# Kernel optimization log

Hardware: AMD Instinct MI355X
Metric: run time of the kernel (lower is better)

## Reference

```python
import jax, jax.numpy as jnp
import numpy as np

N_HEAD = 10

def setup_inputs() -> dict:
    key = jax.random.key(0)
    k1, k2, k3 = jax.random.split(key, 3)
    n_embd = 640
    x = jax.random.normal(k1, (4, 2048, n_embd), dtype=jnp.float32)
    w_qkv = jax.random.normal(k2, (3 * n_embd, n_embd), dtype=jnp.float32) * (1.0 / np.sqrt(n_embd))
    w_proj = jax.random.normal(k3, (n_embd, n_embd), dtype=jnp.float32) * (1.0 / np.sqrt(n_embd))
    return {"x": x, "w_qkv": w_qkv, "w_proj": w_proj}

def reference(x, w_qkv, w_proj):
    bsz, seqlen, n_embd = x.shape
    head_dim = n_embd // N_HEAD
    qkv = jnp.einsum('bsd,ed->bse', x, w_qkv)  # [B,S,3E]
    q, k, v = jnp.split(qkv, 3, axis=2)
    # [B,H,S,Dh]
    q = q.reshape(bsz, seqlen, N_HEAD, head_dim).transpose(0, 2, 1, 3)
    k = k.reshape(bsz, seqlen, N_HEAD, head_dim).transpose(0, 2, 1, 3)
    v = v.reshape(bsz, seqlen, N_HEAD, head_dim).transpose(0, 2, 1, 3)
    scale = 1.0 / np.sqrt(head_dim).astype(np.float32)
    scores = jnp.einsum('bhqd,bhkd->bhqk', q, k) * scale
    causal = jnp.tril(jnp.ones((seqlen, seqlen), dtype=bool))
    scores = jnp.where(causal, scores, jnp.finfo(scores.dtype).min)
    attn = jax.nn.softmax(scores, axis=-1)
    y = jnp.einsum('bhqk,bhkd->bhqd', attn, v)
    y = y.transpose(0, 2, 1, 3).reshape(bsz, seqlen, n_embd)
    return jnp.einsum('bsd,ed->bse', y, w_proj)
```

## Files before the change

kernel.cpp:

```cpp
#include <hip/hip_runtime.h>

#define BB 4
#define SS 2048
#define EE 640
#define NHH 10
#define DHH 64
#define MTOK 8192
#define E33 1920

#define LDST 72

#if __has_builtin(__builtin_amdgcn_exp2f)
#define EXP2(x) __builtin_amdgcn_exp2f(x)
#else
#define EXP2(x) exp2f(x)
#endif

#define QSCALE 0.18033688011112042f

typedef float f32x4 __attribute__((ext_vector_type(4)));
typedef __bf16 bf16x8 __attribute__((ext_vector_type(8)));
typedef __bf16 bf16x4 __attribute__((ext_vector_type(4)));
typedef unsigned short u16;
typedef u16 u16x4 __attribute__((ext_vector_type(4)));

__device__ inline u16 f2bf(float f) {
  unsigned u = __builtin_bit_cast(unsigned, f);
  u += 0x7fffu + ((u >> 16) & 1u);
  return (u16)(u >> 16);
}

#define XN4   1310720
#define WQN4   307200
#define WPN4   102400
__global__ void convert_all(const float* __restrict__ x, const float* __restrict__ wqkv,
                            const float* __restrict__ wproj,
                            u16* __restrict__ xb, u16* __restrict__ wqkvb,
                            u16* __restrict__ wprojb) {
  int i = blockIdx.x * blockDim.x + threadIdx.x;
  const float* src; u16* dst; int off;
  if (i < XN4)              { src = x;     dst = xb;     off = i; }
  else if (i < XN4 + WQN4)  { src = wqkv;  dst = wqkvb;  off = i - XN4; }
  else if (i < XN4 + WQN4 + WPN4) { src = wproj; dst = wprojb; off = i - XN4 - WQN4; }
  else return;
  float4 v = ((const float4*)src)[off];
  u16x4 o = { f2bf(v.x), f2bf(v.y), f2bf(v.z), f2bf(v.w) };
  ((u16x4*)dst)[off] = o;
}

__global__ __launch_bounds__(256) void gemm_qkv(
    const u16* __restrict__ A, const u16* __restrict__ Bt,
    u16* __restrict__ qb, u16* __restrict__ kb, u16* __restrict__ vt) {
  __shared__ __align__(16) u16 As[128 * LDST];
  __shared__ __align__(16) u16 Bs[128 * LDST];
  const int t = threadIdx.x;
  const int m0 = blockIdx.y * 128;
  const int n0 = blockIdx.x * 128;
  const int w = t >> 6, lane = t & 63, n16 = lane & 15, quad = lane >> 4;
  const int wm = w >> 1, wn = w & 1;

  f32x4 acc[4][4];
  for (int i = 0; i < 4; i++)
    for (int j = 0; j < 4; j++) acc[i][j] = f32x4{0.f, 0.f, 0.f, 0.f};

  bf16x8 pa[4], pb[4];
#pragma unroll
  for (int i = 0; i < 4; ++i) {
    int c = i * 256 + t, row = c >> 3, col0 = (c & 7) * 8;
    pa[i] = *(const bf16x8*)&A[(m0 + row) * 640 + col0];
    pb[i] = *(const bf16x8*)&Bt[(n0 + row) * 640 + col0];
  }

  for (int kt = 0; kt < 10; ++kt) {
    __syncthreads();
#pragma unroll
    for (int i = 0; i < 4; ++i) {
      int c = i * 256 + t, row = c >> 3, col0 = (c & 7) * 8;
      *(bf16x8*)&As[row * LDST + col0] = pa[i];
      *(bf16x8*)&Bs[row * LDST + col0] = pb[i];
    }
    __syncthreads();
    if (kt < 9) {
#pragma unroll
      for (int i = 0; i < 4; ++i) {
        int c = i * 256 + t, row = c >> 3, col0 = (c & 7) * 8;
        pa[i] = *(const bf16x8*)&A[(m0 + row) * 640 + (kt + 1) * 64 + col0];
        pb[i] = *(const bf16x8*)&Bt[(n0 + row) * 640 + (kt + 1) * 64 + col0];
      }
    }
#pragma unroll
    for (int ks = 0; ks < 2; ++ks) {
      bf16x8 a[4], b[4];
      for (int mi = 0; mi < 4; mi++)
        a[mi] = *(const bf16x8*)&As[(wm * 64 + mi * 16 + n16) * LDST + ks * 32 + quad * 8];
      for (int ni = 0; ni < 4; ni++)
        b[ni] = *(const bf16x8*)&Bs[(wn * 64 + ni * 16 + n16) * LDST + ks * 32 + quad * 8];
      for (int mi = 0; mi < 4; mi++)
        for (int ni = 0; ni < 4; ni++)
          acc[mi][ni] = __builtin_amdgcn_mfma_f32_16x16x32_bf16(a[mi], b[ni], acc[mi][ni], 0, 0, 0);
    }
  }

  const int which = n0 / 640;
  for (int ni = 0; ni < 4; ni++) {
    int col = n0 + wn * 64 + ni * 16 + n16;
    int eh = col - which * 640;
    int h = eh >> 6, d = eh & 63;
    for (int mi = 0; mi < 4; mi++) {
      int tb = m0 + wm * 64 + mi * 16 + quad * 4;
      f32x4 c = acc[mi][ni];
      if (which == 0) {
        c[0] *= QSCALE; c[1] *= QSCALE; c[2] *= QSCALE; c[3] *= QSCALE;
      }
      if (which == 2) {
        int b_ = tb >> 11, s_ = tb & 2047;
        u16x4 pk = { f2bf(c[0]), f2bf(c[1]), f2bf(c[2]), f2bf(c[3]) };
        *(u16x4*)&vt[((b_ * NHH + h) * DHH + d) * SS + s_] = pk;
      } else {
        u16* dst = (which == 0) ? qb : kb;
        for (int r = 0; r < 4; r++) {
          int tok = tb + r;
          int b_ = tok >> 11, s_ = tok & 2047;
          dst[((b_ * NHH + h) * SS + s_) * DHH + d] = f2bf(c[r]);
        }
      }
    }
  }
}

__global__ __launch_bounds__(256) void attn_kernel(
    const u16* __restrict__ qb, const u16* __restrict__ kb, const u16* __restrict__ vt,
    u16* __restrict__ y) {
  __shared__ __align__(16) u16 Ks[2][64 * LDST];
  __shared__ __align__(16) u16 Vs[2][64 * LDST];
  const int t = threadIdx.x;
  const int w = t >> 6, lane = t & 63, n16 = lane & 15, quad = lane >> 4;
  const int bh = blockIdx.x;
  const int qt = 31 - blockIdx.y;
  const int qb0 = qt * 64;
  const int b_ = bh / NHH, h = bh % NHH;

  bf16x8 aq[2];
  {
    const u16* qp = &qb[(bh * SS + qb0 + w * 16 + n16) * DHH];
    aq[0] = *(const bf16x8*)&qp[quad * 8];
    aq[1] = *(const bf16x8*)&qp[32 + quad * 8];
  }
  const int q_rel = w * 16 + n16;

  const int c1 = 256 + t;
  const int row0 = t >> 3,  col0 = (t & 7) * 8;
  const int row1 = c1 >> 3, col1 = (c1 & 7) * 8;
  auto perm = [](int k) {
    int p = k >> 5, rem = k & 31, qd = rem >> 3, tt = rem & 7;
    return ((p << 1) | (tt >> 2)) * 16 + qd * 4 + (tt & 3);
  };
  const int prow0 = perm(row0), prow1 = perm(row1);

  float4 fk0, fk1, fv0, fv1;
  fk0 = *(const float4*)&kb[(bh * SS + row0) * DHH + col0];
  fk1 = *(const float4*)&kb[(bh * SS + row1) * DHH + col1];
  fv0 = *(const float4*)&vt[(bh * DHH + row0) * SS + col0];
  fv1 = *(const float4*)&vt[(bh * DHH + row1) * SS + col1];
  *(float4*)&Ks[0][prow0 * LDST + col0] = fk0;
  *(float4*)&Ks[0][prow1 * LDST + col1] = fk1;
  *(float4*)&Vs[0][row0 * LDST + col0] = fv0;
  *(float4*)&Vs[0][row1 * LDST + col1] = fv1;

  float m_i = -1e30f, l_i = 0.f;
  f32x4 o[4];
  for (int db = 0; db < 4; db++) o[db] = f32x4{0.f, 0.f, 0.f, 0.f};

  for (int kt = 0; kt <= qt; ++kt) {
    __syncthreads();
    const int cur = kt & 1, nxt = cur ^ 1;
    if (kt < qt) {
      int kk = (kt + 1) * 64;
      fk0 = *(const float4*)&kb[(bh * SS + kk + row0) * DHH + col0];
      fk1 = *(const float4*)&kb[(bh * SS + kk + row1) * DHH + col1];
      fv0 = *(const float4*)&vt[(bh * DHH + row0) * SS + kk + col0];
      fv1 = *(const float4*)&vt[(bh * DHH + row1) * SS + kk + col1];
    }

    f32x4 sc[4];
#pragma unroll
    for (int nb = 0; nb < 4; nb++) {
      f32x4 c = f32x4{0.f, 0.f, 0.f, 0.f};
      bf16x8 ak0 = *(const bf16x8*)&Ks[cur][(nb * 16 + n16) * LDST + quad * 8];
      c = __builtin_amdgcn_mfma_f32_16x16x32_bf16(ak0, aq[0], c, 0, 0, 0);
      bf16x8 ak1 = *(const bf16x8*)&Ks[cur][(nb * 16 + n16) * LDST + 32 + quad * 8];
      c = __builtin_amdgcn_mfma_f32_16x16x32_bf16(ak1, aq[1], c, 0, 0, 0);
      sc[nb] = c;
    }

    if (kt == qt) {
#pragma unroll
      for (int nb = 0; nb < 4; nb++)
#pragma unroll
        for (int r = 0; r < 4; r++) {
          int key = ((nb >> 1) << 5) + quad * 8 + ((nb & 1) << 2) + r;
          if (key > q_rel) sc[nb][r] = -1e30f;
        }
    }

    f32x4 mx;
#pragma unroll
    for (int r = 0; r < 4; r++)
      mx[r] = fmaxf(fmaxf(sc[0][r], sc[1][r]), fmaxf(sc[2][r], sc[3][r]));
    float rm = fmaxf(fmaxf(mx[0], mx[1]), fmaxf(mx[2], mx[3]));
    rm = fmaxf(rm, __shfl_xor(rm, 16));
    rm = fmaxf(rm, __shfl_xor(rm, 32));

    if (!__all(rm - m_i <= 8.0f)) {
      float mnew = fmaxf(m_i, rm);
      float alpha = EXP2(m_i - mnew);
      l_i *= alpha;
#pragma unroll
      for (int db = 0; db < 4; db++)
#pragma unroll
        for (int r = 0; r < 4; r++) o[db][r] *= alpha;
      m_i = mnew;
    }

    f32x4 ps[4];
#pragma unroll
    for (int nb = 0; nb < 4; nb++)
#pragma unroll
      for (int r = 0; r < 4; r++) ps[nb][r] = EXP2(sc[nb][r] - m_i);
    f32x4 sv;
#pragma unroll
    for (int r = 0; r < 4; r++)
      sv[r] = (ps[0][r] + ps[1][r]) + (ps[2][r] + ps[3][r]);
    float rs = (sv[0] + sv[1]) + (sv[2] + sv[3]);
    rs += __shfl_xor(rs, 16);
    rs += __shfl_xor(rs, 32);
    l_i += rs;

#pragma unroll
    for (int p2 = 0; p2 < 2; p2++) {
      bf16x8 bp;
#pragma unroll
      for (int j = 0; j < 4; j++) {
        bp[j]     = (__bf16)ps[2 * p2][j];
        bp[4 + j] = (__bf16)ps[2 * p2 + 1][j];
      }
#pragma unroll
      for (int db = 0; db < 4; db++) {
        bf16x8 av = *(const bf16x8*)&Vs[cur][(db * 16 + n16) * LDST + p2 * 32 + quad * 8];
        o[db] = __builtin_amdgcn_mfma_f32_16x16x32_bf16(av, bp, o[db], 0, 0, 0);
      }
    }

    if (kt < qt) {
      *(float4*)&Ks[nxt][prow0 * LDST + col0] = fk0;
      *(float4*)&Ks[nxt][prow1 * LDST + col1] = fk1;
      *(float4*)&Vs[nxt][row0 * LDST + col0] = fv0;
      *(float4*)&Vs[nxt][row1 * LDST + col1] = fv1;
    }
  }

  const float inv = 1.0f / l_i;
  const int tok = b_ * SS + qb0 + w * 16 + n16;
#pragma unroll
  for (int db = 0; db < 4; db++) {
    bf16x4 pk = { (__bf16)(o[db][0] * inv), (__bf16)(o[db][1] * inv),
                  (__bf16)(o[db][2] * inv), (__bf16)(o[db][3] * inv) };
    *(bf16x4*)&y[tok * EE + h * DHH + db * 16 + quad * 4] = pk;
  }
}

__global__ __launch_bounds__(256) void gemm_proj(
    const u16* __restrict__ A, const u16* __restrict__ Bt, float* __restrict__ out) {
  __shared__ __align__(16) u16 As[128 * LDST];
  __shared__ __align__(16) u16 Bs[128 * LDST];
  const int t = threadIdx.x;
  const int m0 = blockIdx.y * 128;
  const int n0 = blockIdx.x * 128;
  const int w = t >> 6, lane = t & 63, n16 = lane & 15, quad = lane >> 4;
  const int wm = w >> 1, wn = w & 1;

  f32x4 acc[4][4];
  for (int i = 0; i < 4; i++)
    for (int j = 0; j < 4; j++) acc[i][j] = f32x4{0.f, 0.f, 0.f, 0.f};

  bf16x8 pa[4], pb[4];
#pragma unroll
  for (int i = 0; i < 4; ++i) {
    int c = i * 256 + t, row = c >> 3, col0 = (c & 7) * 8;
    pa[i] = *(const bf16x8*)&A[(m0 + row) * 640 + col0];
    pb[i] = *(const bf16x8*)&Bt[(n0 + row) * 640 + col0];
  }

  for (int kt = 0; kt < 10; ++kt) {
    __syncthreads();
#pragma unroll
    for (int i = 0; i < 4; ++i) {
      int c = i * 256 + t, row = c >> 3, col0 = (c & 7) * 8;
      *(bf16x8*)&As[row * LDST + col0] = pa[i];
      *(bf16x8*)&Bs[row * LDST + col0] = pb[i];
    }
    __syncthreads();
    if (kt < 9) {
#pragma unroll
      for (int i = 0; i < 4; ++i) {
        int c = i * 256 + t, row = c >> 3, col0 = (c & 7) * 8;
        pa[i] = *(const bf16x8*)&A[(m0 + row) * 640 + (kt + 1) * 64 + col0];
        pb[i] = *(const bf16x8*)&Bt[(n0 + row) * 640 + (kt + 1) * 64 + col0];
      }
    }
#pragma unroll
    for (int ks = 0; ks < 2; ++ks) {
      bf16x8 a[4], b[4];
      for (int mi = 0; mi < 4; mi++)
        a[mi] = *(const bf16x8*)&As[(wm * 64 + mi * 16 + n16) * LDST + ks * 32 + quad * 8];
      for (int ni = 0; ni < 4; ni++)
        b[ni] = *(const bf16x8*)&Bs[(wn * 64 + ni * 16 + n16) * LDST + ks * 32 + quad * 8];
      for (int mi = 0; mi < 4; mi++)
        for (int ni = 0; ni < 4; ni++)
          acc[mi][ni] = __builtin_amdgcn_mfma_f32_16x16x32_bf16(a[mi], b[ni], acc[mi][ni], 0, 0, 0);
    }
  }

  for (int ni = 0; ni < 4; ni++) {
    int col = n0 + wn * 64 + ni * 16 + n16;
    for (int mi = 0; mi < 4; mi++) {
      int rowb = m0 + wm * 64 + mi * 16 + quad * 4;
      f32x4 c = acc[mi][ni];
      for (int r = 0; r < 4; r++) out[(rowb + r) * 640 + col] = c[r];
    }
  }
}

extern "C" void kernel_launch(void* const* d_in, const int* in_sizes, int n_in,
                              void* d_out, int out_size, void* d_ws, size_t ws_size,
                              hipStream_t stream) {
  const float* x     = (const float*)d_in[0];
  const float* wqkv  = (const float*)d_in[1];
  const float* wproj = (const float*)d_in[2];
  float* out = (float*)d_out;

  char* ws = (char*)d_ws;
  u16* xb     = (u16*)(ws + 0);
  u16* wqkvb  = (u16*)(ws + 10485760);
  u16* wprojb = (u16*)(ws + 12943360);
  u16* qbuf   = (u16*)(ws + 13762560);
  u16* kbuf   = (u16*)(ws + 24248320);
  u16* vtb    = (u16*)(ws + 34734080);
  u16* ybuf   = (u16*)(ws + 45219840);

  convert_all<<<6720, 256, 0, stream>>>(x, wqkv, wproj, xb, wqkvb, wprojb);

  gemm_qkv<<<dim3(15, 64), 256, 0, stream>>>(xb, wqkvb, qbuf, kbuf, vtb);
  attn_kernel<<<dim3(40, 32), 256, 0, stream>>>(qbuf, kbuf, vtb, ybuf);
  gemm_proj<<<dim3(5, 64), 256, 0, stream>>>(ybuf, wprojb, out);
}
```

Measured before the change: 173.5 us.

## Use 128-row query tiles for late causal blocks to reuse K/V tiles

The attention grid becomes a mix of two block types. The first 8 y-blocks each handle a 128-query tile, the upper half of the sequence, with every wave owning 32 query rows, so each K/V tile loaded into shared memory feeds twice as many MFMAs. The remaining 16 blocks keep the old 64-query path for the lower half. This cuts K/V global and LDS traffic and the block count for the heaviest causal tiles, at the cost of more registers per thread and less balanced per-block work.

Measured after the change: 182.6 us. 1.05x slower.

```diff
diff --git a/kernel.cpp b/kernel.cpp
--- a/kernel.cpp
+++ b/kernel.cpp
@@ -136,17 +136,8 @@
   const int t = threadIdx.x;
   const int w = t >> 6, lane = t & 63, n16 = lane & 15, quad = lane >> 4;
   const int bh = blockIdx.x;
-  const int qt = 31 - blockIdx.y;
-  const int qb0 = qt * 64;
+  const int by = blockIdx.y;
   const int b_ = bh / NHH, h = bh % NHH;
-
-  bf16x8 aq[2];
-  {
-    const u16* qp = &qb[(bh * SS + qb0 + w * 16 + n16) * DHH];
-    aq[0] = *(const bf16x8*)&qp[quad * 8];
-    aq[1] = *(const bf16x8*)&qp[32 + quad * 8];
-  }
-  const int q_rel = w * 16 + n16;
 
   const int c1 = 256 + t;
   const int row0 = t >> 3,  col0 = (t & 7) * 8;
@@ -167,105 +158,254 @@
   *(float4*)&Vs[0][row0 * LDST + col0] = fv0;
   *(float4*)&Vs[0][row1 * LDST + col1] = fv1;
 
-  float m_i = -1e30f, l_i = 0.f;
-  f32x4 o[4];
-  for (int db = 0; db < 4; db++) o[db] = f32x4{0.f, 0.f, 0.f, 0.f};
-
-  for (int kt = 0; kt <= qt; ++kt) {
-    __syncthreads();
-    const int cur = kt & 1, nxt = cur ^ 1;
-    if (kt < qt) {
-      int kk = (kt + 1) * 64;
-      fk0 = *(const float4*)&kb[(bh * SS + kk + row0) * DHH + col0];
-      fk1 = *(const float4*)&kb[(bh * SS + kk + row1) * DHH + col1];
-      fv0 = *(const float4*)&vt[(bh * DHH + row0) * SS + kk + col0];
-      fv1 = *(const float4*)&vt[(bh * DHH + row1) * SS + kk + col1];
-    }
-
-    f32x4 sc[4];
-#pragma unroll
-    for (int nb = 0; nb < 4; nb++) {
-      f32x4 c = f32x4{0.f, 0.f, 0.f, 0.f};
-      bf16x8 ak0 = *(const bf16x8*)&Ks[cur][(nb * 16 + n16) * LDST + quad * 8];
-      c = __builtin_amdgcn_mfma_f32_16x16x32_bf16(ak0, aq[0], c, 0, 0, 0);
-      bf16x8 ak1 = *(const bf16x8*)&Ks[cur][(nb * 16 + n16) * LDST + 32 + quad * 8];
-      c = __builtin_amdgcn_mfma_f32_16x16x32_bf16(ak1, aq[1], c, 0, 0, 0);
-      sc[nb] = c;
-    }
-
-    if (kt == qt) {
+  if (by < 8) {
+    const int qt = 15 - by;
+    const int qb0 = qt * 128;
+    const int qlo = w * 32;
+
+    bf16x8 aq[2][2];
+#pragma unroll
+    for (int qh = 0; qh < 2; qh++) {
+      const u16* qp = &qb[(bh * SS + qb0 + qlo + qh * 16 + n16) * DHH];
+      aq[qh][0] = *(const bf16x8*)&qp[quad * 8];
+      aq[qh][1] = *(const bf16x8*)&qp[32 + quad * 8];
+    }
+
+    float m_i[2] = {-1e30f, -1e30f}, l_i[2] = {0.f, 0.f};
+    f32x4 o[2][4];
+#pragma unroll
+    for (int qh = 0; qh < 2; qh++)
+      for (int db = 0; db < 4; db++) o[qh][db] = f32x4{0.f, 0.f, 0.f, 0.f};
+
+    const int nt = 2 * qt + 2;
+
+    for (int kt = 0; kt < nt; ++kt) {
+      __syncthreads();
+      const int cur = kt & 1, nxt = cur ^ 1;
+      if (kt < nt - 1) {
+        int kk = (kt + 1) * 64;
+        fk0 = *(const float4*)&kb[(bh * SS + kk + row0) * DHH + col0];
+        fk1 = *(const float4*)&kb[(bh * SS + kk + row1) * DHH + col1];
+        fv0 = *(const float4*)&vt[(bh * DHH + row0) * SS + kk + col0];
+        fv1 = *(const float4*)&vt[(bh * DHH + row1) * SS + kk + col1];
+      }
+
+      f32x4 sc[2][4];
+#pragma unroll
+      for (int nb = 0; nb < 4; nb++) {
+        f32x4 c0 = f32x4{0.f, 0.f, 0.f, 0.f};
+        f32x4 c1v = f32x4{0.f, 0.f, 0.f, 0.f};
+#pragma unroll
+        for (int ks = 0; ks < 2; ks++) {
+          bf16x8 ak = *(const bf16x8*)&Ks[cur][(nb * 16 + n16) * LDST + ks * 32 + quad * 8];
+          c0 = __builtin_amdgcn_mfma_f32_16x16x32_bf16(ak, aq[0][ks], c0, 0, 0, 0);
+          c1v = __builtin_amdgcn_mfma_f32_16x16x32_bf16(ak, aq[1][ks], c1v, 0, 0, 0);
+        }
+        sc[0][nb] = c0; sc[1][nb] = c1v;
+      }
+
+      const int koff = kt * 64 - 128 * qt;
+      f32x4 ps[2][4];
+      bf16x8 bp[2][2];
+#pragma unroll
+      for (int qh = 0; qh < 2; qh++) {
+        if (koff + 63 > qlo + qh * 16) {
+          const int qrel = qlo + qh * 16 + n16;
+#pragma unroll
+          for (int nb = 0; nb < 4; nb++)
+#pragma unroll
+            for (int r = 0; r < 4; r++) {
+              int key = koff + ((nb >> 1) << 5) + quad * 8 + ((nb & 1) << 2) + r;
+              if (key > qrel) sc[qh][nb][r] = -1e30f;
+            }
+        }
+
+        f32x4 mx;
+#pragma unroll
+        for (int r = 0; r < 4; r++)
+          mx[r] = fmaxf(fmaxf(sc[qh][0][r], sc[qh][1][r]), fmaxf(sc[qh][2][r], sc[qh][3][r]));
+        float rm = fmaxf(fmaxf(mx[0], mx[1]), fmaxf(mx[2], mx[3]));
+        rm = fmaxf(rm, __shfl_xor(rm, 16));
+        rm = fmaxf(rm, __shfl_xor(rm, 32));
+
+        if (!__all(rm - m_i[qh] <= 8.0f)) {
+          float mnew = fmaxf(m_i[qh], rm);
+          float alpha = EXP2(m_i[qh] - mnew);
+          l_i[qh] *= alpha;
+#pragma unroll
+          for (int db = 0; db < 4; db++)
+#pragma unroll
+            for (int r = 0; r < 4; r++) o[qh][db][r] *= alpha;
+          m_i[qh] = mnew;
+        }
+
+#pragma unroll
+        for (int nb = 0; nb < 4; nb++)
+#pragma unroll
+          for (int r = 0; r < 4; r++) ps[qh][nb][r] = EXP2(sc[qh][nb][r] - m_i[qh]);
+        f32x4 sv;
+#pragma unroll
+        for (int r = 0; r < 4; r++)
+          sv[r] = (ps[qh][0][r] + ps[qh][1][r]) + (ps[qh][2][r] + ps[qh][3][r]);
+        float rs = (sv[0] + sv[1]) + (sv[2] + sv[3]);
+        rs += __shfl_xor(rs, 16);
+        rs += __shfl_xor(rs, 32);
+        l_i[qh] += rs;
+
+#pragma unroll
+        for (int p2 = 0; p2 < 2; p2++) {
+          bf16x8 bpv;
+#pragma unroll
+          for (int j = 0; j < 4; j++) {
+            bpv[j]     = (__bf16)ps[qh][2 * p2][j];
+            bpv[4 + j] = (__bf16)ps[qh][2 * p2 + 1][j];
+          }
+          bp[qh][p2] = bpv;
+        }
+      }
+
+#pragma unroll
+      for (int p2 = 0; p2 < 2; p2++) {
+#pragma unroll
+        for (int db = 0; db < 4; db++) {
+          bf16x8 av = *(const bf16x8*)&Vs[cur][(db * 16 + n16) * LDST + p2 * 32 + quad * 8];
+          o[0][db] = __builtin_amdgcn_mfma_f32_16x16x32_bf16(av, bp[0][p2], o[0][db], 0, 0, 0);
+          o[1][db] = __builtin_amdgcn_mfma_f32_16x16x32_bf16(av, bp[1][p2], o[1][db], 0, 0, 0);
+        }
+      }
+
+      if (kt < nt - 1) {
+        *(float4*)&Ks[nxt][prow0 * LDST + col0] = fk0;
+        *(float4*)&Ks[nxt][prow1 * LDST + col1] = fk1;
+        *(float4*)&Vs[nxt][row0 * LDST + col0] = fv0;
+        *(float4*)&Vs[nxt][row1 * LDST + col1] = fv1;
+      }
+    }
+
+#pragma unroll
+    for (int qh = 0; qh < 2; qh++) {
+      const float inv = 1.0f / l_i[qh];
+      const int tok = b_ * SS + qb0 + qlo + qh * 16 + n16;
+#pragma unroll
+      for (int db = 0; db < 4; db++) {
+        bf16x4 pk = { (__bf16)(o[qh][db][0] * inv), (__bf16)(o[qh][db][1] * inv),
+                      (__bf16)(o[qh][db][2] * inv), (__bf16)(o[qh][db][3] * inv) };
+        *(bf16x4*)&y[tok * EE + h * DHH + db * 16 + quad * 4] = pk;
+      }
+    }
+
+  } else {
+    const int qt = 23 - by;
+    const int qb0 = qt * 64;
+
+    bf16x8 aq[2];
+    {
+      const u16* qp = &qb[(bh * SS + qb0 + w * 16 + n16) * DHH];
+      aq[0] = *(const bf16x8*)&qp[quad * 8];
+      aq[1] = *(const bf16x8*)&qp[32 + quad * 8];
+    }
+    const int q_rel = w * 16 + n16;
+
+    float m_i = -1e30f, l_i = 0.f;
+    f32x4 o[4];
+    for (int db = 0; db < 4; db++) o[db] = f32x4{0.f, 0.f, 0.f, 0.f};
+
+    for (int kt = 0; kt <= qt; ++kt) {
+      __syncthreads();
+      const int cur = kt & 1, nxt = cur ^ 1;
+      if (kt < qt) {
+        int kk = (kt + 1) * 64;
+        fk0 = *(const float4*)&kb[(bh * SS + kk + row0) * DHH + col0];
+        fk1 = *(const float4*)&kb[(bh * SS + kk + row1) * DHH + col1];
+        fv0 = *(const float4*)&vt[(bh * DHH + row0) * SS + kk + col0];
+        fv1 = *(const float4*)&vt[(bh * DHH + row1) * SS + kk + col1];
+      }
+
+      f32x4 sc[4];
+#pragma unroll
+      for (int nb = 0; nb < 4; nb++) {
+        f32x4 c = f32x4{0.f, 0.f, 0.f, 0.f};
+        bf16x8 ak0 = *(const bf16x8*)&Ks[cur][(nb * 16 + n16) * LDST + quad * 8];
+        c = __builtin_amdgcn_mfma_f32_16x16x32_bf16(ak0, aq[0], c, 0, 0, 0);
+        bf16x8 ak1 = *(const bf16x8*)&Ks[cur][(nb * 16 + n16) * LDST + 32 + quad * 8];
+        c = __builtin_amdgcn_mfma_f32_16x16x32_bf16(ak1, aq[1], c, 0, 0, 0);
+        sc[nb] = c;
+      }
+
+      if (kt == qt) {
+#pragma unroll
+        for (int nb = 0; nb < 4; nb++)
+#pragma unroll
+          for (int r = 0; r < 4; r++) {
+            int key = ((nb >> 1) << 5) + quad * 8 + ((nb & 1) << 2) + r;
+            if (key > q_rel) sc[nb][r] = -1e30f;
+          }
+      }
+
+      f32x4 mx;
+#pragma unroll
+      for (int r = 0; r < 4; r++)
+        mx[r] = fmaxf(fmaxf(sc[0][r], sc[1][r]), fmaxf(sc[2][r], sc[3][r]));
+      float rm = fmaxf(fmaxf(mx[0], mx[1]), fmaxf(mx[2], mx[3]));
+      rm = fmaxf(rm, __shfl_xor(rm, 16));
+      rm = fmaxf(rm, __shfl_xor(rm, 32));
+
+      if (!__all(rm - m_i <= 8.0f)) {
+        float mnew = fmaxf(m_i, rm);
+        float alpha = EXP2(m_i - mnew);
+        l_i *= alpha;
+#pragma unroll
+        for (int db = 0; db < 4; db++)
+#pragma unroll
+          for (int r = 0; r < 4; r++) o[db][r] *= alpha;
+        m_i = mnew;
+      }
+
+      f32x4 ps[4];
 #pragma unroll
       for (int nb = 0; nb < 4; nb++)
 #pragma unroll
-        for (int r = 0; r < 4; r++) {
-          int key = ((nb >> 1) << 5) + quad * 8 + ((nb & 1) << 2) + r;
-          if (key > q_rel) sc[nb][r] = -1e30f;
-        }
-    }
-
-    f32x4 mx;
-#pragma unroll
-    for (int r = 0; r < 4; r++)
-      mx[r] = fmaxf(fmaxf(sc[0][r], sc[1][r]), fmaxf(sc[2][r], sc[3][r]));
-    float rm = fmaxf(fmaxf(mx[0], mx[1]), fmaxf(mx[2], mx[3]));
-    rm = fmaxf(rm, __shfl_xor(rm, 16));
-    rm = fmaxf(rm, __shfl_xor(rm, 32));
-
-    if (!__all(rm - m_i <= 8.0f)) {
-      float mnew = fmaxf(m_i, rm);
-      float alpha = EXP2(m_i - mnew);
-      l_i *= alpha;
-#pragma unroll
-      for (int db = 0; db < 4; db++)
-#pragma unroll
-        for (int r = 0; r < 4; r++) o[db][r] *= alpha;
-      m_i = mnew;
-    }
-
-    f32x4 ps[4];
-#pragma unroll
-    for (int nb = 0; nb < 4; nb++)
-#pragma unroll
-      for (int r = 0; r < 4; r++) ps[nb][r] = EXP2(sc[nb][r] - m_i);
-    f32x4 sv;
-#pragma unroll
-    for (int r = 0; r < 4; r++)
-      sv[r] = (ps[0][r] + ps[1][r]) + (ps[2][r] + ps[3][r]);
-    float rs = (sv[0] + sv[1]) + (sv[2] + sv[3]);
-    rs += __shfl_xor(rs, 16);
-    rs += __shfl_xor(rs, 32);
-    l_i += rs;
-
-#pragma unroll
-    for (int p2 = 0; p2 < 2; p2++) {
-      bf16x8 bp;
-#pragma unroll
-      for (int j = 0; j < 4; j++) {
-        bp[j]     = (__bf16)ps[2 * p2][j];
-        bp[4 + j] = (__bf16)ps[2 * p2 + 1][j];
-      }
-#pragma unroll
-      for (int db = 0; db < 4; db++) {
-        bf16x8 av = *(const bf16x8*)&Vs[cur][(db * 16 + n16) * LDST + p2 * 32 + quad * 8];
-        o[db] = __builtin_amdgcn_mfma_f32_16x16x32_bf16(av, bp, o[db], 0, 0, 0);
-      }
-    }
-
-    if (kt < qt) {
-      *(float4*)&Ks[nxt][prow0 * LDST + col0] = fk0;
-      *(float4*)&Ks[nxt][prow1 * LDST + col1] = fk1;
-      *(float4*)&Vs[nxt][row0 * LDST + col0] = fv0;
-      *(float4*)&Vs[nxt][row1 * LDST + col1] = fv1;
-    }
-  }
-
-  const float inv = 1.0f / l_i;
-  const int tok = b_ * SS + qb0 + w * 16 + n16;
-#pragma unroll
-  for (int db = 0; db < 4; db++) {
-    bf16x4 pk = { (__bf16)(o[db][0] * inv), (__bf16)(o[db][1] * inv),
-                  (__bf16)(o[db][2] * inv), (__bf16)(o[db][3] * inv) };
-    *(bf16x4*)&y[tok * EE + h * DHH + db * 16 + quad * 4] = pk;
+        for (int r = 0; r < 4; r++) ps[nb][r] = EXP2(sc[nb][r] - m_i);
+      f32x4 sv;
+#pragma unroll
+      for (int r = 0; r < 4; r++)
+        sv[r] = (ps[0][r] + ps[1][r]) + (ps[2][r] + ps[3][r]);
+      float rs = (sv[0] + sv[1]) + (sv[2] + sv[3]);
+      rs += __shfl_xor(rs, 16);
+      rs += __shfl_xor(rs, 32);
+      l_i += rs;
+
+#pragma unroll
+      for (int p2 = 0; p2 < 2; p2++) {
+        bf16x8 bp;
+#pragma unroll
+        for (int j = 0; j < 4; j++) {
+          bp[j]     = (__bf16)ps[2 * p2][j];
+          bp[4 + j] = (__bf16)ps[2 * p2 + 1][j];
+        }
+#pragma unroll
+        for (int db = 0; db < 4; db++) {
+          bf16x8 av = *(const bf16x8*)&Vs[cur][(db * 16 + n16) * LDST + p2 * 32 + quad * 8];
+          o[db] = __builtin_amdgcn_mfma_f32_16x16x32_bf16(av, bp, o[db], 0, 0, 0);
+        }
+      }
+
+      if (kt < qt) {
+        *(float4*)&Ks[nxt][prow0 * LDST + col0] = fk0;
+        *(float4*)&Ks[nxt][prow1 * LDST + col1] = fk1;
+        *(float4*)&Vs[nxt][row0 * LDST + col0] = fv0;
+        *(float4*)&Vs[nxt][row1 * LDST + col1] = fv1;
+      }
+    }
+
+    const float inv = 1.0f / l_i;
+    const int tok = b_ * SS + qb0 + w * 16 + n16;
+#pragma unroll
+    for (int db = 0; db < 4; db++) {
+      bf16x4 pk = { (__bf16)(o[db][0] * inv), (__bf16)(o[db][1] * inv),
+                    (__bf16)(o[db][2] * inv), (__bf16)(o[db][3] * inv) };
+      *(bf16x4*)&y[tok * EE + h * DHH + db * 16 + quad * 4] = pk;
+    }
   }
 }
 
@@ -351,6 +491,6 @@
   convert_all<<<6720, 256, 0, stream>>>(x, wqkv, wproj, xb, wqkvb, wprojb);
 
   gemm_qkv<<<dim3(15, 64), 256, 0, stream>>>(xb, wqkvb, qbuf, kbuf, vtb);
-  attn_kernel<<<dim3(40, 32), 256, 0, stream>>>(qbuf, kbuf, vtb, ybuf);
+  attn_kernel<<<dim3(40, 24), 256, 0, stream>>>(qbuf, kbuf, vtb, ybuf);
   gemm_proj<<<dim3(5, 64), 256, 0, stream>>>(ybuf, wprojb, out);
 }
```

## Load GEMM tiles directly into LDS with XOR-swizzled layout

Applied to the files above, without the earlier changes.

Both projection GEMMs stop staging tiles through registers. Each k-tile is now loaded with global_load_lds (16-byte direct-to-LDS loads) into an unpadded 64-wide tile, and an XOR swizzle replaces the padding to avoid bank conflicts on the MFMA operand reads. This removes the register round-trip and the padded layout, but it also drops the register prefetch of the next tile, so global loads no longer overlap with compute within a block.

Result: slower. 179.5 us (+3.4%).

```diff
diff --git a/kernel.cpp b/kernel.cpp
--- a/kernel.cpp
+++ b/kernel.cpp
@@ -28,6 +28,12 @@
   unsigned u = __builtin_bit_cast(unsigned, f);
   u += 0x7fffu + ((u >> 16) & 1u);
   return (u16)(u >> 16);
+}
+
+__device__ __forceinline__ void gl_lds16(const u16* g, u16* l) {
+  __builtin_amdgcn_global_load_lds(
+      (const __attribute__((address_space(1))) unsigned int*)g,
+      (__attribute__((address_space(3))) unsigned int*)l, 16, 0, 0);
 }
 
 #define XN4   1310720
@@ -51,50 +57,42 @@
 __global__ __launch_bounds__(256) void gemm_qkv(
     const u16* __restrict__ A, const u16* __restrict__ Bt,
     u16* __restrict__ qb, u16* __restrict__ kb, u16* __restrict__ vt) {
-  __shared__ __align__(16) u16 As[128 * LDST];
-  __shared__ __align__(16) u16 Bs[128 * LDST];
+  __shared__ __align__(16) u16 As[128 * 64];
+  __shared__ __align__(16) u16 Bs[128 * 64];
   const int t = threadIdx.x;
   const int m0 = blockIdx.y * 128;
   const int n0 = blockIdx.x * 128;
   const int w = t >> 6, lane = t & 63, n16 = lane & 15, quad = lane >> 4;
   const int wm = w >> 1, wn = w & 1;
 
+  const int sub = lane >> 3, cL = lane & 7;
+  const int srcColE = (cL ^ sub) * 8;
+
+  const int rd0 = (quad ^ (n16 & 7)) * 8;
+  const int rd1 = ((4 + quad) ^ (n16 & 7)) * 8;
+
   f32x4 acc[4][4];
   for (int i = 0; i < 4; i++)
     for (int j = 0; j < 4; j++) acc[i][j] = f32x4{0.f, 0.f, 0.f, 0.f};
 
-  bf16x8 pa[4], pb[4];
-#pragma unroll
-  for (int i = 0; i < 4; ++i) {
-    int c = i * 256 + t, row = c >> 3, col0 = (c & 7) * 8;
-    pa[i] = *(const bf16x8*)&A[(m0 + row) * 640 + col0];
-    pb[i] = *(const bf16x8*)&Bt[(n0 + row) * 640 + col0];
-  }
-
   for (int kt = 0; kt < 10; ++kt) {
     __syncthreads();
 #pragma unroll
     for (int i = 0; i < 4; ++i) {
-      int c = i * 256 + t, row = c >> 3, col0 = (c & 7) * 8;
-      *(bf16x8*)&As[row * LDST + col0] = pa[i];
-      *(bf16x8*)&Bs[row * LDST + col0] = pb[i];
-    }
-    __syncthreads();
-    if (kt < 9) {
-#pragma unroll
-      for (int i = 0; i < 4; ++i) {
-        int c = i * 256 + t, row = c >> 3, col0 = (c & 7) * 8;
-        pa[i] = *(const bf16x8*)&A[(m0 + row) * 640 + (kt + 1) * 64 + col0];
-        pb[i] = *(const bf16x8*)&Bt[(n0 + row) * 640 + (kt + 1) * 64 + col0];
-      }
-    }
+      int c = w * 4 + i;
+      int row = c * 8 + sub;
+      gl_lds16(&A[(m0 + row) * 640 + kt * 64 + srcColE], &As[c * 512]);
+      gl_lds16(&Bt[(n0 + row) * 640 + kt * 64 + srcColE], &Bs[c * 512]);
+    }
+    __syncthreads();
 #pragma unroll
     for (int ks = 0; ks < 2; ++ks) {
+      const int rd = ks ? rd1 : rd0;
       bf16x8 a[4], b[4];
       for (int mi = 0; mi < 4; mi++)
-        a[mi] = *(const bf16x8*)&As[(wm * 64 + mi * 16 + n16) * LDST + ks * 32 + quad * 8];
+        a[mi] = *(const bf16x8*)&As[(wm * 64 + mi * 16 + n16) * 64 + rd];
       for (int ni = 0; ni < 4; ni++)
-        b[ni] = *(const bf16x8*)&Bs[(wn * 64 + ni * 16 + n16) * LDST + ks * 32 + quad * 8];
+        b[ni] = *(const bf16x8*)&Bs[(wn * 64 + ni * 16 + n16) * 64 + rd];
       for (int mi = 0; mi < 4; mi++)
         for (int ni = 0; ni < 4; ni++)
           acc[mi][ni] = __builtin_amdgcn_mfma_f32_16x16x32_bf16(a[mi], b[ni], acc[mi][ni], 0, 0, 0);
@@ -271,50 +269,41 @@
 
 __global__ __launch_bounds__(256) void gemm_proj(
     const u16* __restrict__ A, const u16* __restrict__ Bt, float* __restrict__ out) {
-  __shared__ __align__(16) u16 As[128 * LDST];
-  __shared__ __align__(16) u16 Bs[128 * LDST];
+  __shared__ __align__(16) u16 As[128 * 64];
+  __shared__ __align__(16) u16 Bs[128 * 64];
   const int t = threadIdx.x;
   const int m0 = blockIdx.y * 128;
   const int n0 = blockIdx.x * 128;
   const int w = t >> 6, lane = t & 63, n16 = lane & 15, quad = lane >> 4;
   const int wm = w >> 1, wn = w & 1;
 
+  const int sub = lane >> 3, cL = lane & 7;
+  const int srcColE = (cL ^ sub) * 8;
+  const int rd0 = (quad ^ (n16 & 7)) * 8;
+  const int rd1 = ((4 + quad) ^ (n16 & 7)) * 8;
+
   f32x4 acc[4][4];
   for (int i = 0; i < 4; i++)
     for (int j = 0; j < 4; j++) acc[i][j] = f32x4{0.f, 0.f, 0.f, 0.f};
 
-  bf16x8 pa[4], pb[4];
-#pragma unroll
-  for (int i = 0; i < 4; ++i) {
-    int c = i * 256 + t, row = c >> 3, col0 = (c & 7) * 8;
-    pa[i] = *(const bf16x8*)&A[(m0 + row) * 640 + col0];
-    pb[i] = *(const bf16x8*)&Bt[(n0 + row) * 640 + col0];
-  }
-
   for (int kt = 0; kt < 10; ++kt) {
     __syncthreads();
 #pragma unroll
     for (int i = 0; i < 4; ++i) {
-      int c = i * 256 + t, row = c >> 3, col0 = (c & 7) * 8;
-      *(bf16x8*)&As[row * LDST + col0] = pa[i];
-      *(bf16x8*)&Bs[row * LDST + col0] = pb[i];
-    }
-    __syncthreads();
-    if (kt < 9) {
-#pragma unroll
-      for (int i = 0; i < 4; ++i) {
-        int c = i * 256 + t, row = c >> 3, col0 = (c & 7) * 8;
-        pa[i] = *(const bf16x8*)&A[(m0 + row) * 640 + (kt + 1) * 64 + col0];
-        pb[i] = *(const bf16x8*)&Bt[(n0 + row) * 640 + (kt + 1) * 64 + col0];
-      }
-    }
+      int c = w * 4 + i;
+      int row = c * 8 + sub;
+      gl_lds16(&A[(m0 + row) * 640 + kt * 64 + srcColE], &As[c * 512]);
+      gl_lds16(&Bt[(n0 + row) * 640 + kt * 64 + srcColE], &Bs[c * 512]);
+    }
+    __syncthreads();
 #pragma unroll
     for (int ks = 0; ks < 2; ++ks) {
+      const int rd = ks ? rd1 : rd0;
       bf16x8 a[4], b[4];
       for (int mi = 0; mi < 4; mi++)
-        a[mi] = *(const bf16x8*)&As[(wm * 64 + mi * 16 + n16) * LDST + ks * 32 + quad * 8];
+        a[mi] = *(const bf16x8*)&As[(wm * 64 + mi * 16 + n16) * 64 + rd];
       for (int ni = 0; ni < 4; ni++)
-        b[ni] = *(const bf16x8*)&Bs[(wn * 64 + ni * 16 + n16) * LDST + ks * 32 + quad * 8];
+        b[ni] = *(const bf16x8*)&Bs[(wn * 64 + ni * 16 + n16) * 64 + rd];
       for (int mi = 0; mi < 4; mi++)
         for (int ni = 0; ni < 4; ni++)
           acc[mi][ni] = __builtin_amdgcn_mfma_f32_16x16x32_bf16(a[mi], b[ni], acc[mi][ni], 0, 0, 0);
```
